# Kernel tuning notes

Hardware: AMD Instinct MI355X
Metric: run time of the kernel (lower is better)

The kernel has to match this reference:

```python
import jax, jax.numpy as jnp
import numpy as np

B, S, E, H = 4, 2048, 1024, 16
D = E // H  # per-head dim
SCALE = float(1.0 / np.sqrt(D))


def setup_inputs() -> dict:
    key = jax.random.key(0)
    k1, k2, k3 = jax.random.split(key, 3)
    x = jax.random.normal(k1, (B, S, E), dtype=jnp.float32)
    # xavier_uniform for torch Linear weights (shape [out, in])
    lim_qkv = float(np.sqrt(6.0 / (E + 3 * E)))
    w_qkv = jax.random.uniform(k2, (3 * E, E), minval=-lim_qkv, maxval=lim_qkv, dtype=jnp.float32)
    lim_o = float(np.sqrt(6.0 / (E + E)))
    w_o = jax.random.uniform(k3, (E, E), minval=-lim_o, maxval=lim_o, dtype=jnp.float32)
    return {"x": x, "w_qkv": w_qkv, "w_o": w_o}


def reference(x, w_qkv, w_o):
    b, s, e = x.shape
    # self-attention projection: (b,s,3E) -> (b,s,H,3D) -> chunk into q,k,v
    qkv = (x @ w_qkv.T).reshape(b, s, H, 3 * D)
    q, k, v = jnp.split(qkv, 3, axis=-1)           # each (b,s,H,D)
    q = q.transpose(0, 2, 1, 3)                    # (b,H,s,D)
    k = k.transpose(0, 2, 1, 3)
    v = v.transpose(0, 2, 1, 3)
    logits = jnp.einsum("bhsd,bhtd->bhst", q, k) * SCALE  # (b,H,s,s)
    # NOTE: faithful to source bug — values use raw scaled logits, not softmax(logits)
    values = jnp.einsum("bhst,bhtd->bhsd", logits, v)     # (b,H,s,D)
    values = values.transpose(0, 2, 1, 3).reshape(b, s, e)
    return values @ w_o.T
```

## Files before the change

### kernel.cpp

```cpp
#include <hip/hip_runtime.h>
#include <hip/hip_bf16.h>
#include <cstdint>

#define SCALE_F 0.125f

typedef __attribute__((ext_vector_type(8))) short bf16x8;
typedef __attribute__((ext_vector_type(4))) float f32x4;
typedef __attribute__((ext_vector_type(4))) unsigned short u16x4;
typedef __attribute__((ext_vector_type(8))) unsigned short u16x8;

typedef const __attribute__((address_space(1))) void glb_void;
typedef __attribute__((address_space(3))) void lds_void;

static __device__ __forceinline__ unsigned short f2bf(float f) {
  unsigned u = __builtin_bit_cast(unsigned, f);
  u = (u + 0x7fffu + ((u >> 16) & 1u)) >> 16;
  return (unsigned short)u;
}
static __device__ __forceinline__ float bf2f(unsigned short s) {
  unsigned u = ((unsigned)s) << 16;
  return __builtin_bit_cast(float, u);
}

static __device__ __forceinline__ int xcd_work(int bid, int nwg) {
  int cpx = nwg >> 3;
  return (bid & 7) * cpx + (bid >> 3);
}

__global__ __launch_bounds__(256) void prep(const float* __restrict__ x,
                                            const float* __restrict__ wqkv,
                                            const float* __restrict__ wo,
                                            unsigned short* __restrict__ xb,
                                            unsigned short* __restrict__ xT,
                                            unsigned short* __restrict__ wqt,
                                            unsigned short* __restrict__ wk,
                                            unsigned short* __restrict__ wv,
                                            unsigned short* __restrict__ wob) {
  __shared__ unsigned short lds[64][72];
  const int t = threadIdx.x;
  const int bid = blockIdx.x;

  if (bid < 2048) {
    const int r0 = (bid & 127) * 64, c0 = (bid >> 7) * 64;
#pragma unroll
    for (int pass = 0; pass < 4; ++pass) {
      int r = pass * 16 + (t >> 4);
      int c = (t & 15) * 4;
      float4 v = *(const float4*)(x + (size_t)(r0 + r) * 1024 + c0 + c);
      u16x4 o = { f2bf(v.x), f2bf(v.y), f2bf(v.z), f2bf(v.w) };
      *(u16x4*)(xb + (size_t)(r0 + r) * 1024 + c0 + c) = o;
#pragma unroll
      for (int j = 0; j < 4; ++j) {
        int C = c + j;
        lds[C][r ^ ((C & 7) << 3)] = o[j];
      }
    }
    __syncthreads();
#pragma unroll
    for (int pass = 0; pass < 2; ++pass) {
      int rr = pass * 32 + (t >> 3);
      int cc = (t & 7) * 8;
      u16x8 v = *(const u16x8*)&lds[rr][cc ^ ((rr & 7) << 3)];
      *(u16x8*)(xT + (size_t)(c0 + rr) * 8192 + r0 + cc) = v;
    }
  } else if (bid < 5120) {
    int row = bid - 2048;
    const float* src;
    unsigned short* dst;
    if (row < 1024) {
      int h = row >> 6, k = row & 63;
      src = wqkv + (size_t)(h * 192 + 64 + k) * 1024;
      dst = wk + (size_t)row * 1024;
    } else if (row < 2048) {
      int local = row - 1024;
      int h = local >> 6, k = local & 63;
      src = wqkv + (size_t)(h * 192 + 128 + k) * 1024;
      dst = wv + (size_t)local * 1024;
    } else {
      int local = row - 2048;
      src = wo + (size_t)local * 1024;
      dst = wob + (size_t)local * 1024;
    }
    float4 v = *(const float4*)(src + t * 4);
    u16x4 o = { f2bf(v.x), f2bf(v.y), f2bf(v.z), f2bf(v.w) };
    *(u16x4*)(dst + t * 4) = o;
  } else {
    int tid = bid - 5120;
    const int r0 = (tid & 15) * 64, c0 = (tid >> 4) * 64;
#pragma unroll
    for (int pass = 0; pass < 4; ++pass) {
      int r = pass * 16 + (t >> 4);
      int c = (t & 15) * 4;
      int gr = r0 + r;
      int srcRow = (gr >> 6) * 192 + (gr & 63);
      float4 v = *(const float4*)(wqkv + (size_t)srcRow * 1024 + c0 + c);
      lds[c + 0][r] = f2bf(v.x);
      lds[c + 1][r] = f2bf(v.y);
      lds[c + 2][r] = f2bf(v.z);
      lds[c + 3][r] = f2bf(v.w);
    }
    __syncthreads();
#pragma unroll
    for (int pass = 0; pass < 2; ++pass) {
      int rr = pass * 32 + (t >> 3);
      int cc = (t & 7) * 8;
      *(u16x8*)(wqt + (size_t)(c0 + rr) * 1024 + r0 + cc) = *(const u16x8*)&lds[rr][cc];
    }
  }
}

template<bool F32OUT>
__global__ __launch_bounds__(512) void gemm_bt(const unsigned short* __restrict__ A, int lda,
                                               long aB, long aP,
                                               const unsigned short* __restrict__ Bm, int ldb,
                                               long bB, long bP,
                                               void* __restrict__ Cv, int ldc,
                                               long cB, long cP,
                                               int K, int psplit, int nx, int ny) {
  __shared__ __align__(16) unsigned short Ash[2][128 * 32];
  __shared__ __align__(16) unsigned short Bsh[2][128 * 32];
  const int work = xcd_work(blockIdx.x, gridDim.x);
  const int xt = work % nx;
  const int yt = (work / nx) % ny;
  const int z  = work / (nx * ny);
  const int bb = z / psplit, pp = z % psplit;
  A  += (size_t)bb * aB + (size_t)pp * aP;
  Bm += (size_t)bb * bB + (size_t)pp * bP;
  const int t = threadIdx.x;
  const int w = t >> 6, l = t & 63;
  const int lr = l & 15, lk = l >> 4;
  const int m0 = yt * 128, n0 = xt * 128;
  const int wr = (w >> 2) * 64, wc = (w & 3) * 32;
  const int srow = t >> 2;
  const int skc = ((t & 3) ^ ((srow >> 1) & 3)) << 3;
  const size_t aOff = (size_t)(m0 + srow) * lda + skc;
  const size_t bOff = (size_t)(n0 + srow) * ldb + skc;
  const int fxor = ((lk ^ ((lr >> 1) & 3)) << 3);
  f32x4 acc[4][2] = {};

  __builtin_amdgcn_global_load_lds((glb_void*)(A + aOff), (lds_void*)(Ash[0] + w * 512), 16, 0, 0);
  __builtin_amdgcn_global_load_lds((glb_void*)(Bm + bOff), (lds_void*)(Bsh[0] + w * 512), 16, 0, 0);
  __syncthreads();

  int cur = 0;
  for (int k0 = 0; k0 < K; k0 += 32, cur ^= 1) {
    if (k0 + 32 < K) {
      __builtin_amdgcn_global_load_lds((glb_void*)(A + aOff + k0 + 32),
                                       (lds_void*)(Ash[cur ^ 1] + w * 512), 16, 0, 0);
      __builtin_amdgcn_global_load_lds((glb_void*)(Bm + bOff + k0 + 32),
                                       (lds_void*)(Bsh[cur ^ 1] + w * 512), 16, 0, 0);
    }
    bf16x8 af[4], bfv[2];
#pragma unroll
    for (int mi = 0; mi < 4; ++mi)
      af[mi] = *(const bf16x8*)(Ash[cur] + (wr + mi * 16 + lr) * 32 + fxor);
#pragma unroll
    for (int ni = 0; ni < 2; ++ni)
      bfv[ni] = *(const bf16x8*)(Bsh[cur] + (wc + ni * 16 + lr) * 32 + fxor);
#pragma unroll
    for (int mi = 0; mi < 4; ++mi)
#pragma unroll
      for (int ni = 0; ni < 2; ++ni)
        acc[mi][ni] = __builtin_amdgcn_mfma_f32_16x16x32_bf16(af[mi], bfv[ni], acc[mi][ni], 0, 0, 0);
    __syncthreads();
  }

#pragma unroll
  for (int mi = 0; mi < 4; ++mi)
#pragma unroll
    for (int ni = 0; ni < 2; ++ni)
#pragma unroll
      for (int r = 0; r < 4; ++r) {
        const size_t row = (size_t)(m0 + wr + mi * 16 + lk * 4 + r);
        const size_t col = (size_t)(n0 + wc + ni * 16 + lr);
        if constexpr (F32OUT)
          ((float*)Cv)[(size_t)bb * cB + (size_t)pp * cP + row * ldc + col] = acc[mi][ni][r];
        else
          ((unsigned short*)Cv)[(size_t)bb * cB + (size_t)pp * cP + row * ldc + col] = f2bf(acc[mi][ni][r]);
      }
}

__global__ __launch_bounds__(512) void gemm_tri(const unsigned short* __restrict__ xT,
                                                unsigned short* __restrict__ Gp) {
  __shared__ __align__(16) unsigned short Ash[2][128 * 32];
  __shared__ __align__(16) unsigned short Bsh[2][128 * 32];
  const int work = xcd_work(blockIdx.x, gridDim.x);
  int ti = work % 36;
  const int z = work / 36;
  int mt = 0, accum = 0;
  while (accum + mt + 1 <= ti) { accum += mt + 1; ++mt; }
  int nt = ti - accum;
  const int b = z >> 2, p = z & 3;
  const unsigned short* base = xT + (size_t)b * 2048 + (size_t)p * 512;

  const int t = threadIdx.x;
  const int w = t >> 6, l = t & 63;
  const int lr = l & 15, lk = l >> 4;
  const int m0 = mt * 128, n0 = nt * 128;
  const int wr = (w >> 2) * 64, wc = (w & 3) * 32;
  const int srow = t >> 2;
  const int skc = ((t & 3) ^ ((srow >> 1) & 3)) << 3;
  const size_t aOff = (size_t)(m0 + srow) * 8192 + skc;
  const size_t bOff = (size_t)(n0 + srow) * 8192 + skc;
  const int fxor = ((lk ^ ((lr >> 1) & 3)) << 3);
  f32x4 acc[4][2] = {};

  __builtin_amdgcn_global_load_lds((glb_void*)(base + aOff), (lds_void*)(Ash[0] + w * 512), 16, 0, 0);
  __builtin_amdgcn_global_load_lds((glb_void*)(base + bOff), (lds_void*)(Bsh[0] + w * 512), 16, 0, 0);
  __syncthreads();

  int cur = 0;
  for (int k0 = 0; k0 < 512; k0 += 32, cur ^= 1) {
    if (k0 + 32 < 512) {
      __builtin_amdgcn_global_load_lds((glb_void*)(base + aOff + k0 + 32),
                                       (lds_void*)(Ash[cur ^ 1] + w * 512), 16, 0, 0);
      __builtin_amdgcn_global_load_lds((glb_void*)(base + bOff + k0 + 32),
                                       (lds_void*)(Bsh[cur ^ 1] + w * 512), 16, 0, 0);
    }
    bf16x8 af[4], bfv[2];
#pragma unroll
    for (int mi = 0; mi < 4; ++mi)
      af[mi] = *(const bf16x8*)(Ash[cur] + (wr + mi * 16 + lr) * 32 + fxor);
#pragma unroll
    for (int ni = 0; ni < 2; ++ni)
      bfv[ni] = *(const bf16x8*)(Bsh[cur] + (wc + ni * 16 + lr) * 32 + fxor);
#pragma unroll
    for (int mi = 0; mi < 4; ++mi)
#pragma unroll
      for (int ni = 0; ni < 2; ++ni)
        acc[mi][ni] = __builtin_amdgcn_mfma_f32_16x16x32_bf16(af[mi], bfv[ni], acc[mi][ni], 0, 0, 0);
    __syncthreads();
  }

  unsigned short* out = Gp + (size_t)z * 1048576;
#pragma unroll
  for (int mi = 0; mi < 4; ++mi)
#pragma unroll
    for (int ni = 0; ni < 2; ++ni)
#pragma unroll
      for (int r = 0; r < 4; ++r)
        out[(size_t)(m0 + wr + mi * 16 + lk * 4 + r) * 1024 + n0 + wc + ni * 16 + lr]
            = f2bf(acc[mi][ni][r]);
}

__global__ __launch_bounds__(256) void mirror_reduce(const unsigned short* __restrict__ Gp,
                                                     unsigned short* __restrict__ G) {
  __shared__ unsigned short ldsT[128][128];
  int ti = blockIdx.x;
  int mt = 0, accum = 0;
  while (accum + mt + 1 <= ti) { accum += mt + 1; ++mt; }
  int nt = ti - accum;
  const int b = blockIdx.y;
  const int m0 = mt * 128, n0 = nt * 128;
  const unsigned short* base = Gp + (size_t)b * 4 * 1048576;
  unsigned short* Gb = G + (size_t)b * 1048576;
  const int t = threadIdx.x;

#pragma unroll
  for (int pass = 0; pass < 8; ++pass) {
    int idx = pass * 2048 + t * 8;
    int r = idx >> 7, c = idx & 127;
    float s[8] = {};
#pragma unroll
    for (int p = 0; p < 4; ++p) {
      u16x8 v = *(const u16x8*)(base + (size_t)p * 1048576 + (size_t)(m0 + r) * 1024 + n0 + c);
#pragma unroll
      for (int j = 0; j < 8; ++j) s[j] += bf2f(v[j]);
    }
    u16x8 o;
#pragma unroll
    for (int j = 0; j < 8; ++j) o[j] = f2bf(s[j]);
    *(u16x8*)(Gb + (size_t)(m0 + r) * 1024 + n0 + c) = o;
#pragma unroll
    for (int j = 0; j < 8; ++j) {
      int col = c + j;
      ldsT[col][r ^ (((col >> 3) & 7) << 3)] = o[j];
    }
  }

  if (mt != nt) {
    __syncthreads();
#pragma unroll
    for (int pass = 0; pass < 8; ++pass) {
      int idx = pass * 2048 + t * 8;
      int rr = idx >> 7, cc = idx & 127;
      u16x8 v = *(const u16x8*)&ldsT[rr][cc ^ (((rr >> 3) & 7) << 3)];
      *(u16x8*)(Gb + (size_t)(n0 + rr) * 1024 + m0 + cc) = v;
    }
  }
}

__global__ __launch_bounds__(256) void mt_partial(const unsigned short* __restrict__ T1p,
                                                  const unsigned short* __restrict__ wv,
                                                  float* __restrict__ Mp) {
  __shared__ float Msh[4096];
  const int t = threadIdx.x;
  const int w = t >> 6, l = t & 63;
  const int lr = l & 15, lk = l >> 4;
  const int bh = blockIdx.x, ep = blockIdx.y;
  const int b = bh >> 4, h = bh & 15;
  const int p = w >> 1, half = w & 1;

  for (int i = t; i < 4096; i += 256) Msh[i] = 0.f;
  __syncthreads();

  const unsigned short* Ab = T1p + (size_t)(b * 2 + p) * 1048576 + (size_t)(h * 64) * 1024;
  const unsigned short* Bb = wv + (size_t)(h * 64) * 1024;
  f32x4 acc[4][4] = {};
  const int ebeg = ep * 256 + half * 128;
#pragma unroll
  for (int e0 = ebeg; e0 < ebeg + 128; e0 += 32) {
    bf16x8 af[4], bfv[4];
#pragma unroll
    for (int mi = 0; mi < 4; ++mi)
      af[mi] = *(const bf16x8*)(Ab + (size_t)(mi * 16 + lr) * 1024 + e0 + lk * 8);
#pragma unroll
    for (int ni = 0; ni < 4; ++ni)
      bfv[ni] = *(const bf16x8*)(Bb + (size_t)(ni * 16 + lr) * 1024 + e0 + lk * 8);
#pragma unroll
    for (int mi = 0; mi < 4; ++mi)
#pragma unroll
      for (int ni = 0; ni < 4; ++ni)
        acc[mi][ni] = __builtin_amdgcn_mfma_f32_16x16x32_bf16(af[mi], bfv[ni], acc[mi][ni], 0, 0, 0);
  }
#pragma unroll
  for (int mi = 0; mi < 4; ++mi)
#pragma unroll
    for (int ni = 0; ni < 4; ++ni)
#pragma unroll
      for (int r = 0; r < 4; ++r)
        atomicAdd(&Msh[(mi * 16 + lk * 4 + r) * 64 + ni * 16 + lr], acc[mi][ni][r]);
  __syncthreads();

  float* out = Mp + ((size_t)bh * 4 + ep) * 4096;
  for (int i = t * 4; i < 4096; i += 1024)
    *(float4*)(out + i) = *(const float4*)&Msh[i];
}

__global__ __launch_bounds__(256) void amat_fused(const float* __restrict__ Mp,
                                                  const unsigned short* __restrict__ wqt,
                                                  unsigned short* __restrict__ Amat) {
  __shared__ float Msh[64 * 68];
  __shared__ unsigned short MtSh[64][80];
  const int t = threadIdx.x;
  const int et = blockIdx.x, bh = blockIdx.y;
  const int b = bh >> 4, h = bh & 15;

  const float* base = Mp + (size_t)bh * 16384;
  for (int i = t * 4; i < 4096; i += 1024) {
    float4 s = *(const float4*)(base + i);
#pragma unroll
    for (int p = 1; p < 4; ++p) {
      float4 v = *(const float4*)(base + p * 4096 + i);
      s.x += v.x; s.y += v.y; s.z += v.z; s.w += v.w;
    }
    int k = i >> 6, dp = i & 63;
    *(float4*)&Msh[k * 68 + dp] = s;
  }
  __syncthreads();

  for (int i = t; i < 4096; i += 256) {
    int dp = i >> 6, k = i & 63;
    MtSh[dp][k] = f2bf(Msh[k * 68 + dp] * SCALE_F);
  }
  __syncthreads();

  const int w = t >> 6, l = t & 63;
  const int lr = l & 15, lk = l >> 4;
  const int e0 = et * 128 + w * 32;

  f32x4 acc[2][4] = {};
#pragma unroll
  for (int ks = 0; ks < 2; ++ks) {
    bf16x8 af[2], bfv[4];
#pragma unroll
    for (int mi = 0; mi < 2; ++mi)
      af[mi] = *(const bf16x8*)(wqt + (size_t)(e0 + mi * 16 + lr) * 1024 + h * 64 + ks * 32 + lk * 8);
#pragma unroll
    for (int ni = 0; ni < 4; ++ni)
      bfv[ni] = *(const bf16x8*)(&MtSh[ni * 16 + lr][ks * 32 + lk * 8]);
#pragma unroll
    for (int mi = 0; mi < 2; ++mi)
#pragma unroll
      for (int ni = 0; ni < 4; ++ni)
        acc[mi][ni] = __builtin_amdgcn_mfma_f32_16x16x32_bf16(af[mi], bfv[ni], acc[mi][ni], 0, 0, 0);
  }
#pragma unroll
  for (int mi = 0; mi < 2; ++mi)
#pragma unroll
    for (int ni = 0; ni < 4; ++ni)
#pragma unroll
      for (int r = 0; r < 4; ++r)
        Amat[(size_t)b * 1048576 + (size_t)(e0 + mi * 16 + lk * 4 + r) * 1024 + h * 64 + ni * 16 + lr]
            = f2bf(acc[mi][ni][r]);
}

extern "C" void kernel_launch(void* const* d_in, const int* in_sizes, int n_in,
                              void* d_out, int out_size, void* d_ws, size_t ws_size,
                              hipStream_t stream) {
  const float* x    = (const float*)d_in[0];
  const float* wqkv = (const float*)d_in[1];
  const float* wo   = (const float*)d_in[2];
  float* out = (float*)d_out;

  char* ws = (char*)d_ws;
  const size_t MB = 1048576;
  unsigned short* xb   = (unsigned short*)(ws + 0);
  unsigned short* xT   = (unsigned short*)(ws + 16 * MB);
  unsigned short* wqt  = (unsigned short*)(ws + 32 * MB);
  unsigned short* wk   = (unsigned short*)(ws + 34 * MB);
  unsigned short* wv   = (unsigned short*)(ws + 36 * MB);
  unsigned short* wob  = (unsigned short*)(ws + 38 * MB);
  unsigned short* Gp   = (unsigned short*)(ws + 40 * MB);
  unsigned short* G    = (unsigned short*)(ws + 72 * MB);
  unsigned short* T1p  = (unsigned short*)(ws + 40 * MB);
  float*          Mp   = (float*)        (ws + 56 * MB);
  unsigned short* Amat = (unsigned short*)(ws + 61 * MB);
  unsigned short* Weff = (unsigned short*)(ws + 40 * MB);

  const long M1 = 1048576;

  prep<<<5376, 256, 0, stream>>>(x, wqkv, wo, xb, xT, wqt, wk, wv, wob);

  gemm_tri<<<576, 512, 0, stream>>>(xT, Gp);
  mirror_reduce<<<dim3(36, 4), 256, 0, stream>>>(Gp, G);

  gemm_bt<false><<<512, 512, 0, stream>>>(wk, 1024, 0, 512,
                                          G, 1024, M1, 512,
                                          (void*)T1p, 1024, 2 * M1, M1, 512, 2, 8, 8);

  mt_partial<<<dim3(64, 4), 256, 0, stream>>>(T1p, wv, Mp);

  amat_fused<<<dim3(8, 64), 256, 0, stream>>>(Mp, wqt, Amat);

  gemm_bt<false><<<256, 512, 0, stream>>>(wob, 1024, 0, 0,
                                          Amat, 1024, M1, 0,
                                          (void*)Weff, 1024, M1, 0, 1024, 1, 8, 8);

  gemm_bt<true><<<512, 512, 0, stream>>>(xb, 1024, 2048 * 1024L, 0,
                                         Weff, 1024, M1, 0,
                                         (void*)out, 1024, 2048 * 1024L, 0, 1024, 1, 8, 16);
}
```

Baseline: 145.1 us.

## Fuse wk·G projection and wv contraction into one mdirect kernel

Replaces the separate gemm_bt producing the T1p intermediate and the mt_partial kernel with a single kernel. Each block computes a 64x128 slice of wk·G through double-buffered global_load_lds tiles, keeps it in LDS as bf16, then immediately contracts it with the matching wv slice. The result is written as 8 partial M tiles per (b,h), which amat_fused now sums. This removes a global round trip of the T1p intermediate, one kernel launch, and the shared-memory atomics. In exchange it re-reads G per head, stores the intermediate in bf16, and doubles the partial sums amat_fused must read.

```diff
diff --git a/kernel.cpp b/kernel.cpp
--- a/kernel.cpp
+++ b/kernel.cpp
@@ -290,51 +290,102 @@
   }
 }
 
-__global__ __launch_bounds__(256) void mt_partial(const unsigned short* __restrict__ T1p,
-                                                  const unsigned short* __restrict__ wv,
-                                                  float* __restrict__ Mp) {
-  __shared__ float Msh[4096];
+__global__ __launch_bounds__(512) void mdirect(const unsigned short* __restrict__ wk,
+                                               const unsigned short* __restrict__ G,
+                                               const unsigned short* __restrict__ wv,
+                                               float* __restrict__ Mp) {
+  __shared__ __align__(16) unsigned short Awk[2][64 * 32];
+  __shared__ __align__(16) unsigned short Bg[2][128 * 32];
+  __shared__ __align__(16) unsigned short Ut[64 * 128];
+  __shared__ __align__(16) unsigned short WvS[64 * 128];
+  const int work = xcd_work(blockIdx.x, gridDim.x);
+  const int bh = work >> 3, es = work & 7;
+  const int b = bh >> 4, h = bh & 15;
+  const int e0 = es * 128;
   const int t = threadIdx.x;
   const int w = t >> 6, l = t & 63;
   const int lr = l & 15, lk = l >> 4;
-  const int bh = blockIdx.x, ep = blockIdx.y;
-  const int b = bh >> 4, h = bh & 15;
-  const int p = w >> 1, half = w & 1;
-
-  for (int i = t; i < 4096; i += 256) Msh[i] = 0.f;
-  __syncthreads();
-
-  const unsigned short* Ab = T1p + (size_t)(b * 2 + p) * 1048576 + (size_t)(h * 64) * 1024;
-  const unsigned short* Bb = wv + (size_t)(h * 64) * 1024;
-  f32x4 acc[4][4] = {};
-  const int ebeg = ep * 256 + half * 128;
-#pragma unroll
-  for (int e0 = ebeg; e0 < ebeg + 128; e0 += 32) {
-    bf16x8 af[4], bfv[4];
-#pragma unroll
-    for (int mi = 0; mi < 4; ++mi)
-      af[mi] = *(const bf16x8*)(Ab + (size_t)(mi * 16 + lr) * 1024 + e0 + lk * 8);
+
+  const unsigned short* wkB = wk + (size_t)(h * 64) * 1024;
+  const unsigned short* Gb  = G + (size_t)b * 1048576 + (size_t)e0 * 1024;
+  const unsigned short* wvB = wv + (size_t)(h * 64) * 1024 + e0;
+
+  const int arow = t >> 2, askc = ((t & 3) ^ ((arow >> 1) & 3)) << 3;
+  const int brow = t >> 2, bskc = ((t & 3) ^ ((brow >> 1) & 3)) << 3;
+  const size_t aOff = (size_t)arow * 1024 + askc;
+  const size_t bOff = (size_t)brow * 1024 + bskc;
+  const int fxor = ((lk ^ ((lr >> 1) & 3)) << 3);
+
+#pragma unroll
+  for (int i = 0; i < 2; ++i) {
+    int idx = i * 512 + t;
+    int row = idx >> 4, slot = idx & 15;
+    int sslot = slot ^ (row & 15);
+    __builtin_amdgcn_global_load_lds(
+        (glb_void*)(wvB + (size_t)row * 1024 + sslot * 8),
+        (lds_void*)(WvS + i * 4096 + w * 512), 16, 0, 0);
+  }
+  if (t < 256)
+    __builtin_amdgcn_global_load_lds((glb_void*)(wkB + aOff),
+                                     (lds_void*)(Awk[0] + w * 512), 16, 0, 0);
+  __builtin_amdgcn_global_load_lds((glb_void*)(Gb + bOff),
+                                   (lds_void*)(Bg[0] + w * 512), 16, 0, 0);
+  __syncthreads();
+
+  const int wc = w * 16;
+  f32x4 acc[4] = {};
+  int cur = 0;
+  for (int k0 = 0; k0 < 1024; k0 += 32, cur ^= 1) {
+    if (k0 + 32 < 1024) {
+      if (t < 256)
+        __builtin_amdgcn_global_load_lds((glb_void*)(wkB + aOff + k0 + 32),
+                                         (lds_void*)(Awk[cur ^ 1] + w * 512), 16, 0, 0);
+      __builtin_amdgcn_global_load_lds((glb_void*)(Gb + bOff + k0 + 32),
+                                       (lds_void*)(Bg[cur ^ 1] + w * 512), 16, 0, 0);
+    }
+    bf16x8 af[4], bfv;
+#pragma unroll
+    for (int mi = 0; mi < 4; ++mi)
+      af[mi] = *(const bf16x8*)(Awk[cur] + (mi * 16 + lr) * 32 + fxor);
+    bfv = *(const bf16x8*)(Bg[cur] + (wc + lr) * 32 + fxor);
+#pragma unroll
+    for (int mi = 0; mi < 4; ++mi)
+      acc[mi] = __builtin_amdgcn_mfma_f32_16x16x32_bf16(af[mi], bfv, acc[mi], 0, 0, 0);
+    __syncthreads();
+  }
+
+#pragma unroll
+  for (int mi = 0; mi < 4; ++mi)
+#pragma unroll
+    for (int r = 0; r < 4; ++r) {
+      int i = mi * 16 + lk * 4 + r;
+      int col = wc + lr;
+      int addr = i * 128 + ((((col >> 3) ^ (i & 15)) << 3) | (col & 7));
+      Ut[addr] = f2bf(acc[mi][r]);
+    }
+  __syncthreads();
+
+  if (w < 4) {
+    f32x4 acc2[4] = {};
+#pragma unroll
+    for (int ks = 0; ks < 4; ++ks) {
+      int slot = (ks << 2) | lk;
+      bf16x8 a2 = *(const bf16x8*)(Ut + (w * 16 + lr) * 128 + ((slot ^ lr) << 3));
+      bf16x8 b2[4];
+#pragma unroll
+      for (int ni = 0; ni < 4; ++ni)
+        b2[ni] = *(const bf16x8*)(WvS + (ni * 16 + lr) * 128 + ((slot ^ lr) << 3));
+#pragma unroll
+      for (int ni = 0; ni < 4; ++ni)
+        acc2[ni] = __builtin_amdgcn_mfma_f32_16x16x32_bf16(a2, b2[ni], acc2[ni], 0, 0, 0);
+    }
+    float* out = Mp + ((size_t)bh * 8 + es) * 4096;
 #pragma unroll
     for (int ni = 0; ni < 4; ++ni)
-      bfv[ni] = *(const bf16x8*)(Bb + (size_t)(ni * 16 + lr) * 1024 + e0 + lk * 8);
-#pragma unroll
-    for (int mi = 0; mi < 4; ++mi)
-#pragma unroll
-      for (int ni = 0; ni < 4; ++ni)
-        acc[mi][ni] = __builtin_amdgcn_mfma_f32_16x16x32_bf16(af[mi], bfv[ni], acc[mi][ni], 0, 0, 0);
-  }
-#pragma unroll
-  for (int mi = 0; mi < 4; ++mi)
-#pragma unroll
-    for (int ni = 0; ni < 4; ++ni)
 #pragma unroll
       for (int r = 0; r < 4; ++r)
-        atomicAdd(&Msh[(mi * 16 + lk * 4 + r) * 64 + ni * 16 + lr], acc[mi][ni][r]);
-  __syncthreads();
-
-  float* out = Mp + ((size_t)bh * 4 + ep) * 4096;
-  for (int i = t * 4; i < 4096; i += 1024)
-    *(float4*)(out + i) = *(const float4*)&Msh[i];
+        out[(w * 16 + lk * 4 + r) * 64 + ni * 16 + lr] = acc2[ni][r];
+  }
 }
 
 __global__ __launch_bounds__(256) void amat_fused(const float* __restrict__ Mp,
@@ -346,11 +397,11 @@
   const int et = blockIdx.x, bh = blockIdx.y;
   const int b = bh >> 4, h = bh & 15;
 
-  const float* base = Mp + (size_t)bh * 16384;
+  const float* base = Mp + (size_t)bh * 32768;
   for (int i = t * 4; i < 4096; i += 1024) {
     float4 s = *(const float4*)(base + i);
 #pragma unroll
-    for (int p = 1; p < 4; ++p) {
+    for (int p = 1; p < 8; ++p) {
       float4 v = *(const float4*)(base + p * 4096 + i);
       s.x += v.x; s.y += v.y; s.z += v.z; s.w += v.w;
     }
@@ -413,10 +464,9 @@
   unsigned short* wob  = (unsigned short*)(ws + 38 * MB);
   unsigned short* Gp   = (unsigned short*)(ws + 40 * MB);
   unsigned short* G    = (unsigned short*)(ws + 72 * MB);
-  unsigned short* T1p  = (unsigned short*)(ws + 40 * MB);
-  float*          Mp   = (float*)        (ws + 56 * MB);
-  unsigned short* Amat = (unsigned short*)(ws + 61 * MB);
-  unsigned short* Weff = (unsigned short*)(ws + 40 * MB);
+  float*          Mp   = (float*)        (ws + 40 * MB);
+  unsigned short* Amat = (unsigned short*)(ws + 48 * MB);
+  unsigned short* Weff = (unsigned short*)(ws + 56 * MB);
 
   const long M1 = 1048576;
 
@@ -425,11 +475,7 @@
   gemm_tri<<<576, 512, 0, stream>>>(xT, Gp);
   mirror_reduce<<<dim3(36, 4), 256, 0, stream>>>(Gp, G);
 
-  gemm_bt<false><<<512, 512, 0, stream>>>(wk, 1024, 0, 512,
-                                          G, 1024, M1, 512,
-                                          (void*)T1p, 1024, 2 * M1, M1, 512, 2, 8, 8);
-
-  mt_partial<<<dim3(64, 4), 256, 0, stream>>>(T1p, wv, Mp);
+  mdirect<<<512, 512, 0, stream>>>(wk, G, wv, Mp);
 
   amat_fused<<<dim3(8, 64), 256, 0, stream>>>(Mp, wqt, Amat);
 
```

Result: faster. 122.6 us, median of 2 (-15.5%).
